# Kernel optimization log

Measured on AMD Instinct MI355X. Metric: run time of the kernel, lower is better.

Reference implementation:

```python
import jax, jax.numpy as jnp
import numpy as np

N, M, H = 200000, 400000, 128
EPS = 1e-12  # torch F.normalize eps


def _l2norm(x):
    # F.normalize(x, p=2, dim=-1): x / max(||x||, eps)
    n = jnp.linalg.norm(x, axis=-1, keepdims=True)
    return x / jnp.maximum(n, EPS)


def message_norm(feat, msg, scale):
    # DGL MessageNorm(learn_scale=True): normalize(msg) * ||feat|| * scale
    feat_norm = jnp.linalg.norm(feat, axis=-1, keepdims=True)
    return _l2norm(msg) * feat_norm * scale


def setup_inputs() -> dict:
    key = jax.random.key(0)
    ks = jax.random.split(key, 8)
    h_src = jax.random.normal(ks[0], (M, H), dtype=jnp.float32)
    c_src = jax.random.normal(ks[1], (M, H), dtype=jnp.float32)
    iou = jax.random.normal(ks[2], (N, 3 * H), dtype=jnp.float32)
    child_idx = jax.random.randint(ks[3], (N, 2), 0, M, dtype=jnp.int64)
    # torch nn.Linear layout: y = x @ W.T + b
    lim_f = 1.0 / np.sqrt(2 * H)
    W_f = jax.random.uniform(ks[4], (2 * H, 2 * H), minval=-lim_f, maxval=lim_f, dtype=jnp.float32)
    b_f = jax.random.uniform(ks[5], (2 * H,), minval=-lim_f, maxval=lim_f, dtype=jnp.float32)
    W_iou = jax.random.uniform(ks[6], (3 * H, 2 * H), minval=-lim_f, maxval=lim_f, dtype=jnp.float32)
    b_iou = jnp.zeros((1, 3 * H), dtype=jnp.float32)
    scale_iou = jnp.ones((), dtype=jnp.float32)
    scale_c = jnp.ones((), dtype=jnp.float32)
    return {"h_src": h_src, "c_src": c_src, "iou": iou, "child_idx": child_idx,
            "W_f": W_f, "b_f": b_f, "W_iou": W_iou, "b_iou": b_iou,
            "scale_iou": scale_iou, "scale_c": scale_c}


def reference(h_src, c_src, iou, child_idx, W_f, b_f, W_iou, b_iou, scale_iou, scale_c):
    # --- reduce_func: gather children, forget gates, weighted cell sum ---
    h_ch = h_src[child_idx]                 # [N, 2, H]
    c_ch = c_src[child_idx]                 # [N, 2, H]
    h_cat = h_ch.reshape(h_ch.shape[0], -1)  # [N, 2H]
    f = jax.nn.sigmoid(h_cat @ W_f.T + b_f).reshape(h_ch.shape)  # [N, 2, H]
    c_sum = jnp.sum(f * c_ch, axis=1)       # [N, H]
    iou_n = message_norm(iou, h_cat, scale_iou) @ W_iou.T  # [N, 3H]
    c_dat = message_norm(c_ch[:, 0, :], c_sum, scale_c)    # [N, H]
    # --- apply_node_func ---
    iou_b = iou_n + b_iou
    i, o, u = jnp.split(iou_b, 3, axis=1)
    c = jax.nn.sigmoid(i) * jnp.tanh(u) + c_dat
    h = jax.nn.sigmoid(o) * jnp.tanh(c)
    return jnp.stack([h, c], axis=1)        # [N, 2, H]
```

## Files before the change

### kernel.cpp

```cpp
#include <hip/hip_runtime.h>
#include <math.h>

typedef __attribute__((ext_vector_type(4))) float f32x4;
typedef __attribute__((ext_vector_type(2))) float f32x2;
typedef __attribute__((ext_vector_type(8))) short bf16x8;
typedef __attribute__((ext_vector_type(4))) short short4v;

#define EPSN 1e-12f
#define TN 32
#define FS 268
#define IS 396
#define FBASE 8192
#define UTOT 16768

__device__ inline short f2bf(float x) {
    union { float f; unsigned u; } v; v.f = x;
    unsigned r = v.u + 0x7fffu + ((v.u >> 16) & 1u);
    return (short)(r >> 16);
}
__device__ inline float bf2f(short s) {
    union { unsigned u; float f; } v;
    v.u = ((unsigned)(unsigned short)s) << 16;
    return v.f;
}
__device__ inline float wsum64(float v) {
#pragma unroll
    for (int m = 32; m > 0; m >>= 1) v += __shfl_xor(v, m);
    return v;
}
__device__ inline float wsum32(float v) {
    v += __shfl_xor(v, 1);
    v += __shfl_xor(v, 2);
    v += __shfl_xor(v, 4);
    v += __shfl_xor(v, 8);
    v += __shfl_xor(v, 16);
    return v;
}
__device__ inline float sigm(float x) { return 1.0f / (1.0f + __expf(-x)); }
__device__ inline float tanh_fast(float x) {
    float a = fabsf(x);
    float e = __expf(2.0f * a);
    float t = 1.0f - 2.0f / (e + 1.0f);
    return copysignf(t, x);
}
__device__ inline float dot4(f32x4 v) { return v.x*v.x + v.y*v.y + v.z*v.z + v.w*v.w; }

__global__ void prep_B(const float* __restrict__ W_f, const float* __restrict__ W_iou,
                       short* __restrict__ Blin) {
    int t = blockIdx.x * 256 + threadIdx.x;
    if (t >= 8 * 40 * 64) return;
    int lane = t & 63;
    int jb = (t >> 6) % 40;
    int kb = (t >> 6) / 40;
    int j = jb * 16 + (lane & 15);
    int k = kb * 32 + ((lane >> 4) << 3);
    const float* src = (j < 256) ? (W_f + (size_t)j * 256 + k)
                                 : (W_iou + (size_t)(j - 256) * 256 + k);
    bf16x8 v;
#pragma unroll
    for (int e = 0; e < 8; ++e) v[e] = f2bf(src[e]);
    *(bf16x8*)(Blin + (size_t)t * 8) = v;
}

template<int NJJ>
__device__ inline void gpass32(const short* __restrict__ A, const short* __restrict__ Blin,
                               int lane, int jbase, f32x4 acc[2][NJJ]) {
    const int la = lane & 15, kg = lane >> 4;
#pragma unroll
    for (int kb = 0; kb < 8; ++kb) {
        bf16x8 af[2];
#pragma unroll
        for (int m = 0; m < 2; ++m) {
            const int f = kb * 128 + kg * 32 + m * 16 + la;
            af[m] = *(const bf16x8*)&A[(f ^ ((f >> 5) & 7)) << 3];
        }
#pragma unroll
        for (int jj = 0; jj < NJJ; ++jj) {
            const bf16x8 b = *(const bf16x8*)(Blin +
                ((size_t)((kb * 40 + jbase + jj) * 64 + lane)) * 8);
            acc[0][jj] = __builtin_amdgcn_mfma_f32_16x16x32_bf16(af[0], b, acc[0][jj], 0, 0, 0);
            acc[1][jj] = __builtin_amdgcn_mfma_f32_16x16x32_bf16(af[1], b, acc[1][jj], 0, 0, 0);
        }
    }
}

__global__ __launch_bounds__(512, 4) void tree_fused(
    const float* __restrict__ h_src, const float* __restrict__ c_src,
    const float* __restrict__ iou, const int* __restrict__ child_idx,
    const float* __restrict__ b_f, const float* __restrict__ b_iou,
    const float* __restrict__ sc_iou_p, const float* __restrict__ sc_c_p,
    const short* __restrict__ Blin, float* __restrict__ out) {
    __shared__ __align__(16) short U[UTOT];
    __shared__ float h_n2[TN], iou_n2[TN];
    __shared__ int cc_lds[TN][2];

    const int tid = threadIdx.x;
    const int wave = tid >> 6;
    const int lane = tid & 63;
    const int la = lane & 15, kg = lane >> 4;
    const size_t nb0 = (size_t)blockIdx.x * TN;

    const float sc_iou = sc_iou_p[0];
    const float sc_c = sc_c_p[0];

    const float bf0 = b_f[(wave * 2 + 0) * 16 + la];
    const float bf1 = b_f[(wave * 2 + 1) * 16 + la];

    {
        const int child = lane >> 5;
        const int seg = lane & 31;
        int cix[4];
#pragma unroll
        for (int r = 0; r < 4; ++r)
            cix[r] = child_idx[(size_t)(nb0 + wave + 8 * r) * 2 + child];
        f32x4 hv[4];
#pragma unroll
        for (int r = 0; r < 4; ++r)
            hv[r] = *(const f32x4*)(h_src + (size_t)cix[r] * 128 + seg * 4);
#pragma unroll
        for (int r = 0; r < 4; ++r) {
            const int nd = wave + 8 * r;
            const size_t node = nb0 + nd;
            const int f = (child * 4 + (seg >> 3)) * 128 + ((seg >> 1) & 3) * 32 + nd;
            const int addr = ((f ^ ((f >> 5) & 7)) << 3) + (seg & 1) * 4;
            short4v a4;
            a4.x = f2bf(hv[r].x); a4.y = f2bf(hv[r].y);
            a4.z = f2bf(hv[r].z); a4.w = f2bf(hv[r].w);
            *(short4v*)&U[addr] = a4;
            if (lane == 0) cc_lds[nd][0] = cix[r];
            if (lane == 32) cc_lds[nd][1] = cix[r];
            float hss = wsum64(dot4(hv[r]));
            const f32x4 v4 = *(const f32x4*)(iou + node * 384 + lane * 4);
            const f32x2 v2 = *(const f32x2*)(iou + node * 384 + 256 + lane * 2);
            float iss = wsum64(dot4(v4) + v2.x * v2.x + v2.y * v2.y);
            if (lane == 0) { h_n2[nd] = hss; iou_n2[nd] = iss; }
        }
    }
    __syncthreads();

    const int nd0 = tid >> 5;
    const int q = tid & 31;
    const int h0q = q * 4;

    const int c00 = cc_lds[nd0][0];
    const int c01 = cc_lds[nd0][1];
    const f32x4 c0a = *(const f32x4*)(c_src + (size_t)c00 * 128 + h0q);
    const f32x4 c1a = *(const f32x4*)(c_src + (size_t)c01 * 128 + h0q);

    f32x4 accf[2][2];
    accf[0][0] = (f32x4){bf0, bf0, bf0, bf0};
    accf[1][0] = accf[0][0];
    accf[0][1] = (f32x4){bf1, bf1, bf1, bf1};
    accf[1][1] = accf[0][1];
    gpass32<2>(U, Blin, lane, wave * 2, accf);

    const int c10 = cc_lds[16 + nd0][0];
    const int c11 = cc_lds[16 + nd0][1];
    const f32x4 c0b = *(const f32x4*)(c_src + (size_t)c10 * 128 + h0q);
    const f32x4 c1b = *(const f32x4*)(c_src + (size_t)c11 * 128 + h0q);

#pragma unroll
    for (int m = 0; m < 2; ++m)
#pragma unroll
        for (int jj = 0; jj < 2; ++jj) {
            const int col = (wave * 2 + jj) * 16 + la;
#pragma unroll
            for (int r = 0; r < 4; ++r) {
                const int row = m * 16 + kg * 4 + r;
                U[FBASE + row * FS + col] = f2bf(accf[m][jj][r]);
            }
        }
    __syncthreads();

    f32x4 accio[2][3];
#pragma unroll
    for (int m = 0; m < 2; ++m)
#pragma unroll
        for (int jj = 0; jj < 3; ++jj) accio[m][jj] = (f32x4){0.f, 0.f, 0.f, 0.f};
    gpass32<3>(U, Blin, lane, 16 + wave * 3, accio);

    float csr[2][4], s_v[2];
#pragma unroll
    for (int p = 0; p < 2; ++p) {
        const int nd = p * 16 + nd0;
        const f32x4 c0v = p ? c0b : c0a;
        const f32x4 c1v = p ? c1b : c1a;
        const short4v yf0 = *(const short4v*)&U[FBASE + nd * FS + h0q];
        const short4v yf1 = *(const short4v*)&U[FBASE + nd * FS + 128 + h0q];
        float c0n2 = wsum32(dot4(c0v));
        float cs[4];
        float csn2 = 0.f;
#pragma unroll
        for (int e = 0; e < 4; ++e) {
            const float f0 = sigm(bf2f(yf0[e]));
            const float f1 = sigm(bf2f(yf1[e]));
            const float v = f0 * ((const float*)&c0v)[e] + f1 * ((const float*)&c1v)[e];
            cs[e] = v;
            csn2 += v * v;
        }
        csn2 = wsum32(csn2);
        const float rs = sc_c * sqrtf(c0n2) / fmaxf(sqrtf(csn2), EPSN);
#pragma unroll
        for (int e = 0; e < 4; ++e) csr[p][e] = cs[e] * rs;
        s_v[p] = sc_iou * sqrtf(iou_n2[nd]) / fmaxf(sqrtf(h_n2[nd]), EPSN);
    }
    __syncthreads();

#pragma unroll
    for (int m = 0; m < 2; ++m)
#pragma unroll
        for (int jj = 0; jj < 3; ++jj) {
            const int col = (wave * 3 + jj) * 16 + la;
#pragma unroll
            for (int r = 0; r < 4; ++r) {
                const int row = m * 16 + kg * 4 + r;
                U[row * IS + col] = f2bf(accio[m][jj][r]);
            }
        }
    __syncthreads();

    const f32x4 bi0 = *(const f32x4*)(b_iou + h0q);
    const f32x4 bi1 = *(const f32x4*)(b_iou + 128 + h0q);
    const f32x4 bi2 = *(const f32x4*)(b_iou + 256 + h0q);
#pragma unroll
    for (int p = 0; p < 2; ++p) {
        const int nd = p * 16 + nd0;
        const size_t node = nb0 + nd;
        const short4v yi = *(const short4v*)&U[nd * IS + h0q];
        const short4v yo = *(const short4v*)&U[nd * IS + 128 + h0q];
        const short4v yu = *(const short4v*)&U[nd * IS + 256 + h0q];
        f32x4 outh, outc;
#pragma unroll
        for (int e = 0; e < 4; ++e) {
            const float iv = bf2f(yi[e]) * s_v[p] + ((const float*)&bi0)[e];
            const float ov = bf2f(yo[e]) * s_v[p] + ((const float*)&bi1)[e];
            const float uv = bf2f(yu[e]) * s_v[p] + ((const float*)&bi2)[e];
            const float cval = sigm(iv) * tanh_fast(uv) + csr[p][e];
            const float hval = sigm(ov) * tanh_fast(cval);
            ((float*)&outh)[e] = hval;
            ((float*)&outc)[e] = cval;
        }
        *(f32x4*)(out + node * 256 + h0q) = outh;
        *(f32x4*)(out + node * 256 + 128 + h0q) = outc;
    }
}

extern "C" void kernel_launch(void* const* d_in, const int* in_sizes, int n_in,
                              void* d_out, int out_size, void* d_ws, size_t ws_size,
                              hipStream_t stream) {
    const float* h_src = (const float*)d_in[0];
    const float* c_src = (const float*)d_in[1];
    const float* iou = (const float*)d_in[2];
    const int* cidx = (const int*)d_in[3];
    const float* W_f = (const float*)d_in[4];
    const float* b_f = (const float*)d_in[5];
    const float* W_iou = (const float*)d_in[6];
    const float* b_iou = (const float*)d_in[7];
    const float* s_iou = (const float*)d_in[8];
    const float* s_c = (const float*)d_in[9];
    float* out = (float*)d_out;
    short* Blin = (short*)d_ws;

    const int N = in_sizes[3] / 2;
    const int ntiles = N / TN;
    hipLaunchKernelGGL(prep_B, dim3(80), dim3(256), 0, stream, W_f, W_iou, Blin);
    hipLaunchKernelGGL(tree_fused, dim3(ntiles), dim3(512), 0, stream,
                       h_src, c_src, iou, cidx, b_f, b_iou, s_iou, s_c, Blin, out);
}
```

Baseline: 265.0 us.

## Split iou GEMM into two stages to cut live accumulators and reuse LDS

Breaks the 3-tile iou GEMM pass into a 2-tile pass (i,o) stored to the forget-gate LDS region and a 1-tile pass (u) stored to a smaller region, and moves the forget-gate store and bias loads into a scoped block. The goal is fewer simultaneously live accumulator registers so 4 blocks per CU fit without spills. The cost is an extra barrier and a reordered schedule in which the iou GEMM no longer overlaps the cell-norm computation.

```diff
diff --git a/kernel.cpp b/kernel.cpp
--- a/kernel.cpp
+++ b/kernel.cpp
@@ -9,7 +9,7 @@
 #define EPSN 1e-12f
 #define TN 32
 #define FS 268
-#define IS 396
+#define BS 136
 #define FBASE 8192
 #define UTOT 16768
 
@@ -102,9 +102,6 @@
 
     const float sc_iou = sc_iou_p[0];
     const float sc_c = sc_c_p[0];
-
-    const float bf0 = b_f[(wave * 2 + 0) * 16 + la];
-    const float bf1 = b_f[(wave * 2 + 1) * 16 + la];
 
     {
         const int child = lane >> 5;
@@ -147,37 +144,33 @@
     const f32x4 c0a = *(const f32x4*)(c_src + (size_t)c00 * 128 + h0q);
     const f32x4 c1a = *(const f32x4*)(c_src + (size_t)c01 * 128 + h0q);
 
-    f32x4 accf[2][2];
-    accf[0][0] = (f32x4){bf0, bf0, bf0, bf0};
-    accf[1][0] = accf[0][0];
-    accf[0][1] = (f32x4){bf1, bf1, bf1, bf1};
-    accf[1][1] = accf[0][1];
-    gpass32<2>(U, Blin, lane, wave * 2, accf);
+    {
+        f32x4 accf[2][2];
+        const float bf0 = b_f[(wave * 2 + 0) * 16 + la];
+        const float bf1 = b_f[(wave * 2 + 1) * 16 + la];
+        accf[0][0] = (f32x4){bf0, bf0, bf0, bf0};
+        accf[1][0] = accf[0][0];
+        accf[0][1] = (f32x4){bf1, bf1, bf1, bf1};
+        accf[1][1] = accf[0][1];
+        gpass32<2>(U, Blin, lane, wave * 2, accf);
+#pragma unroll
+        for (int m = 0; m < 2; ++m)
+#pragma unroll
+            for (int jj = 0; jj < 2; ++jj) {
+                const int col = (wave * 2 + jj) * 16 + la;
+#pragma unroll
+                for (int r = 0; r < 4; ++r) {
+                    const int row = m * 16 + kg * 4 + r;
+                    U[FBASE + row * FS + col] = f2bf(accf[m][jj][r]);
+                }
+            }
+    }
 
     const int c10 = cc_lds[16 + nd0][0];
     const int c11 = cc_lds[16 + nd0][1];
     const f32x4 c0b = *(const f32x4*)(c_src + (size_t)c10 * 128 + h0q);
     const f32x4 c1b = *(const f32x4*)(c_src + (size_t)c11 * 128 + h0q);
-
-#pragma unroll
-    for (int m = 0; m < 2; ++m)
-#pragma unroll
-        for (int jj = 0; jj < 2; ++jj) {
-            const int col = (wave * 2 + jj) * 16 + la;
-#pragma unroll
-            for (int r = 0; r < 4; ++r) {
-                const int row = m * 16 + kg * 4 + r;
-                U[FBASE + row * FS + col] = f2bf(accf[m][jj][r]);
-            }
-        }
-    __syncthreads();
-
-    f32x4 accio[2][3];
-#pragma unroll
-    for (int m = 0; m < 2; ++m)
-#pragma unroll
-        for (int jj = 0; jj < 3; ++jj) accio[m][jj] = (f32x4){0.f, 0.f, 0.f, 0.f};
-    gpass32<3>(U, Blin, lane, 16 + wave * 3, accio);
+    __syncthreads();
 
     float csr[2][4], s_v[2];
 #pragma unroll
@@ -206,17 +199,41 @@
     }
     __syncthreads();
 
-#pragma unroll
-    for (int m = 0; m < 2; ++m)
-#pragma unroll
-        for (int jj = 0; jj < 3; ++jj) {
-            const int col = (wave * 3 + jj) * 16 + la;
-#pragma unroll
-            for (int r = 0; r < 4; ++r) {
-                const int row = m * 16 + kg * 4 + r;
-                U[row * IS + col] = f2bf(accio[m][jj][r]);
+    {
+        f32x4 accA[2][2];
+#pragma unroll
+        for (int m = 0; m < 2; ++m)
+#pragma unroll
+            for (int jj = 0; jj < 2; ++jj) accA[m][jj] = (f32x4){0.f, 0.f, 0.f, 0.f};
+        gpass32<2>(U, Blin, lane, 16 + wave * 2, accA);
+#pragma unroll
+        for (int m = 0; m < 2; ++m)
+#pragma unroll
+            for (int jj = 0; jj < 2; ++jj) {
+                const int col = (wave * 2 + jj) * 16 + la;
+#pragma unroll
+                for (int r = 0; r < 4; ++r) {
+                    const int row = m * 16 + kg * 4 + r;
+                    U[FBASE + row * FS + col] = f2bf(accA[m][jj][r]);
+                }
             }
-        }
+    }
+
+    f32x4 accB[2][1];
+    accB[0][0] = (f32x4){0.f, 0.f, 0.f, 0.f};
+    accB[1][0] = accB[0][0];
+    gpass32<1>(U, Blin, lane, 32 + wave, accB);
+    __syncthreads();
+
+#pragma unroll
+    for (int m = 0; m < 2; ++m) {
+        const int col = wave * 16 + la;
+#pragma unroll
+        for (int r = 0; r < 4; ++r) {
+            const int row = m * 16 + kg * 4 + r;
+            U[row * BS + col] = f2bf(accB[m][0][r]);
+        }
+    }
     __syncthreads();
 
     const f32x4 bi0 = *(const f32x4*)(b_iou + h0q);
@@ -226,9 +243,9 @@
     for (int p = 0; p < 2; ++p) {
         const int nd = p * 16 + nd0;
         const size_t node = nb0 + nd;
-        const short4v yi = *(const short4v*)&U[nd * IS + h0q];
-        const short4v yo = *(const short4v*)&U[nd * IS + 128 + h0q];
-        const short4v yu = *(const short4v*)&U[nd * IS + 256 + h0q];
+        const short4v yi = *(const short4v*)&U[FBASE + nd * FS + h0q];
+        const short4v yo = *(const short4v*)&U[FBASE + nd * FS + 128 + h0q];
+        const short4v yu = *(const short4v*)&U[nd * BS + h0q];
         f32x4 outh, outc;
 #pragma unroll
         for (int e = 0; e < 4; ++e) {
```

After: 300.8 us. 13.5% more time.
